# Kernel optimization log

Hardware: AMD Instinct MI355X
Metric: run time of the kernel (lower is better)

Reference implementation:

```python
import jax, jax.numpy as jnp
import numpy as np

B, S, D = 32, 512, 1024  # batch, seq_len, input_dim == output_dim


def setup_inputs() -> dict:
    key = jax.random.key(0)
    ks = jax.random.split(key, 13)
    std = 0.05  # tf.random_normal_initializer default stddev
    w = lambda k, shp: (jax.random.normal(k, shp, dtype=jnp.float32) * std)
    inp = {"seq_input_vec": jax.random.normal(ks[0], (B, S, D), dtype=jnp.float32)}
    names = ["Ui", "Wi", "Uf", "Wf", "Uo", "Wo", "Ug", "Wg"]
    for i, n in enumerate(names):
        inp[n] = w(ks[1 + i], (D, D))
    for n in ["bi", "bf", "bo", "bg"]:
        inp[n] = jnp.zeros((D,), dtype=jnp.float32)
    return inp


def reference(seq_input_vec, Ui, Wi, bi, Uf, Wf, bf, Uo, Wo, bo, Ug, Wg, bg):
    # seq_input_vec: [B, S, D]. Fuse the 4 input projections into one GEMM
    # over the whole sequence (mathematically identical to per-step matmuls).
    U = jnp.concatenate([Ui, Uf, Uo, Ug], axis=1)          # [D, 4D]
    W = jnp.concatenate([Wi, Wf, Wo, Wg], axis=1)          # [D, 4D]
    b = jnp.concatenate([bi, bf, bo, bg], axis=0)          # [4D]
    x_proj = jnp.einsum('bsd,de->sbe', seq_input_vec, U) + b  # [S, B, 4D]

    d = seq_input_vec.shape[-1]
    h0 = jnp.zeros((seq_input_vec.shape[0], d), dtype=seq_input_vec.dtype)
    c0 = jnp.zeros_like(h0)

    def step(carry, xp):
        c_prev, h_prev = carry
        z = xp + h_prev @ W                                 # [B, 4D]
        zi, zf, zo, zg = jnp.split(z, 4, axis=-1)
        i_t = jax.nn.sigmoid(zi)
        f_t = jax.nn.sigmoid(zf)
        o_t = jax.nn.sigmoid(zo)
        g_t = jnp.tanh(zg)
        # NOTE: original (nonstandard) math applies sigmoid to the cell update
        c_t = jax.nn.sigmoid(f_t * c_prev + i_t * g_t)
        h_t = jnp.tanh(c_t) * o_t
        return (c_t, h_t), h_t

    _, hs = jax.lax.scan(step, (c0, h0), x_proj)            # hs: [S, B, D]
    return jnp.transpose(hs, (1, 0, 2))                     # [B, S, D]
```

## Files before the change

### kernel.cpp

```cpp
#include <hip/hip_runtime.h>

typedef unsigned int u32;
typedef unsigned short u16;
typedef unsigned long long u64;
typedef __attribute__((ext_vector_type(8))) short short8;
typedef __attribute__((ext_vector_type(4))) float f32x4;
typedef __attribute__((ext_vector_type(4))) u32 u32x4;

#define SEQ 512
#define BATCH 32
#define DIM 1024
#define NB 128

#define OFF_XT    0ull
#define OFF_UBT   33554432ull
#define OFF_WG2   41943040ull
#define OFF_XPROJ 50331648ull
#define OFF_BIAS  184680448ull
#define OFF_SYNC  184696832ull

__device__ __forceinline__ float bf2f(u16 u) {
  union { u32 u; float f; } v; v.u = ((u32)u) << 16; return v.f;
}
__device__ __forceinline__ u16 f2bf(float f) {
  union { float f; u32 u; } v; v.f = f;
  u32 r = v.u + 0x7FFFu + ((v.u >> 16) & 1u);
  return (u16)(r >> 16);
}
__device__ __forceinline__ float tanh_fast(float x) {
  return 1.f - 2.f / (1.f + __expf(2.f * x));
}
__device__ __forceinline__ void gload_lds16(const u16* g, u16* l) {
  __builtin_amdgcn_global_load_lds(
      (const __attribute__((address_space(1))) u32*)g,
      (__attribute__((address_space(3))) u32*)l, 16, 0, 0);
}
__device__ __forceinline__ void gload_lds16_coh(const u16* g, u16* l) {
  __builtin_amdgcn_global_load_lds(
      (const __attribute__((address_space(1))) u32*)g,
      (__attribute__((address_space(3))) u32*)l, 16, 0, 17);
}

__global__ void k_init(float* biasc, u32* sync, const float* bi,
                       const float* bfv, const float* bo, const float* bg) {
  int i = blockIdx.x * 256 + threadIdx.x;
  if (i < 4096) {
    int g = i >> 10, c = i & 1023;
    const float* p = (g == 0) ? bi : (g == 1) ? bfv : (g == 2) ? bo : bg;
    biasc[i] = p[c];
  } else if (i < 8192) {
    sync[i - 4096] = 0u;
  }
}

__global__ void k_zero(u32x4* p) {
  p[blockIdx.x * 256 + threadIdx.x] = (u32x4){0u, 0u, 0u, 0u};
}

__global__ void k_prep_w(const float* Ui, const float* Wi, const float* Uf,
                         const float* Wf, const float* Uo, const float* Wo,
                         const float* Ug, const float* Wg, u16* Ubt, u16* Wg2) {
  __shared__ float tile[64][65];
  int bx = blockIdx.x;
  int mi = bx >> 8;
  int tt = bx & 255;
  int tr = tt >> 4, tc = tt & 15;
  const float* src;
  switch (mi) {
    case 0: src = Ui; break; case 1: src = Wi; break;
    case 2: src = Uf; break; case 3: src = Wf; break;
    case 4: src = Uo; break; case 5: src = Wo; break;
    case 6: src = Ug; break; default: src = Wg; break;
  }
  int g = mi >> 1;
  int d0 = tr * 64, c0 = tc * 64;
  int ty = threadIdx.x >> 6, tx = threadIdx.x & 63;
#pragma unroll
  for (int i = 0; i < 16; ++i) {
    int r = i * 4 + ty;
    tile[r][tx] = src[(size_t)(d0 + r) * 1024 + c0 + tx];
  }
  __syncthreads();
  if (mi & 1) {
#pragma unroll
    for (int i = 0; i < 16; ++i) {
      int cc = i * 4 + ty;
      int c_full = c0 + cc;
      int k = d0 + tx;
      int blk = c_full >> 3;
      int lane = (((k & 31) >> 3) << 4) + ((c_full & 3) << 2) + g;
      size_t idx = (size_t)blk * 32768 +
                   (size_t)(((k >> 5) * 2 + ((c_full & 7) >> 2)) * 64 + lane) * 8 +
                   (k & 7);
      Wg2[idx] = f2bf(tile[tx][cc]);
    }
  } else {
#pragma unroll
    for (int i = 0; i < 16; ++i) {
      int cc = i * 4 + ty;
      Ubt[(size_t)((g << 10) + c0 + cc) * 1024 + d0 + tx] = f2bf(tile[tx][cc]);
    }
  }
}

__global__ void k_prep_x(const float* __restrict__ X, u16* __restrict__ Xt) {
  int idx = blockIdx.x * 256 + threadIdx.x;
  int m = idx >> 8, d4 = (idx & 255) << 2;
  int s = m >> 5, b = m & 31;
  const float4* p = (const float4*)(X + (size_t)(b * SEQ + s) * DIM + d4);
  float4 v = *p;
  u16 o[4] = { f2bf(v.x), f2bf(v.y), f2bf(v.z), f2bf(v.w) };
  *(ushort4*)(Xt + (size_t)m * DIM + d4) = *(ushort4*)o;
}

__global__ __launch_bounds__(256) void k_gemm(const u16* __restrict__ Xt,
                                              const u16* __restrict__ Ubt,
                                              const float* __restrict__ biasc,
                                              u16* __restrict__ xp2) {
  __shared__ u16 As[128 * 32];
  __shared__ u16 Bs[128 * 32];
  __shared__ u16 cbuf[4][16][8][32];
  int tid = threadIdx.x;
  int w = tid >> 6, l = tid & 63;
  int n0 = blockIdx.x * 128, m0 = blockIdx.y * 128;
  int wm = w >> 1, wn = w & 1;
  int lrow = l & 15, lq = l >> 4;
  f32x4 acc[4][4] = {};
  for (int kt = 0; kt < 32; ++kt) {
    int k0 = kt * 32;
    __syncthreads();
#pragma unroll
    for (int is = 0; is < 2; ++is) {
      int c = is * 256 + w * 64 + l;
      int row = c >> 2, kg = c & 3;
      gload_lds16(Xt + (size_t)(m0 + row) * 1024 + k0 + kg * 8, As + c * 8);
      gload_lds16(Ubt + (size_t)(n0 + row) * 1024 + k0 + kg * 8, Bs + c * 8);
    }
    __syncthreads();
    short8 af[4], bfr[4];
#pragma unroll
    for (int mt = 0; mt < 4; ++mt)
      af[mt] = *(const short8*)(As + (wm * 64 + mt * 16 + lrow) * 32 + lq * 8);
#pragma unroll
    for (int nt = 0; nt < 4; ++nt)
      bfr[nt] = *(const short8*)(Bs + (wn * 64 + nt * 16 + lrow) * 32 + lq * 8);
#pragma unroll
    for (int mt = 0; mt < 4; ++mt)
#pragma unroll
      for (int nt = 0; nt < 4; ++nt)
        acc[mt][nt] = __builtin_amdgcn_mfma_f32_16x16x32_bf16(
            af[mt], bfr[nt], acc[mt][nt], 0, 0, 0);
  }
#pragma unroll
  for (int nt = 0; nt < 4; ++nt) {
    int lc = wn * 64 + nt * 16 + lrow;
    float bv = biasc[n0 + lc];
#pragma unroll
    for (int mt = 0; mt < 4; ++mt) {
#pragma unroll
      for (int r = 0; r < 4; ++r) {
        int lr = wm * 64 + mt * 16 + lq * 4 + r;
        cbuf[lr >> 5][lc >> 3][lrow & 7][lr & 31] = f2bf(acc[mt][nt][r] + bv);
      }
    }
  }
  __syncthreads();
  int s0 = m0 >> 5, blkd0 = (n0 & 1023) >> 3, gb = (n0 >> 10) * 256;
  const u16* cb = &cbuf[0][0][0][0];
#pragma unroll
  for (int i = 0; i < 8; ++i) {
    int u = i * 256 + tid;
    int r_ = u >> 5, w_ = u & 31;
    u32x4 v = *(const u32x4*)(cb + u * 8);
    *(u32x4*)(xp2 + (size_t)((s0 + (r_ >> 4)) * 128 + blkd0 + (r_ & 15)) * 1024 +
              gb + w_ * 8) = v;
  }
}

__global__ __launch_bounds__(256, 1) void k_rec(const u16* __restrict__ Wg2,
                                                const u16* __restrict__ xp2,
                                                u16* hX, const u16* __restrict__ h0,
                                                u32* sync) {
  __shared__ u16 Hs[32768];
  __shared__ u16 XPs[2][1024];
  int tid = threadIdx.x;
  int w = tid >> 6, l = tid & 63;
  int mt = w >> 1, nt = w & 1;
  int blk = blockIdx.x;
  int q = l >> 4, b15 = l & 15;

  short8 wf[32];
#pragma unroll
  for (int kt = 0; kt < 32; ++kt)
    wf[kt] = *(const short8*)(Wg2 + (size_t)blk * 32768 + (kt * 2 + mt) * 512 +
                              l * 8);
  if (tid < 128)
    gload_lds16(xp2 + (size_t)blk * 1024 + tid * 8, XPs[0] + tid * 8);
  asm volatile("s_waitcnt vmcnt(0)" ::: "memory");
  __builtin_amdgcn_sched_barrier(0);

  int hoff = (((blk >> 2) * 2 + nt) * 64 + (blk & 3) * 16 + b15) * 8 + mt * 4 + q;
  int xoff = (mt * 4 + q) * 32 + nt * 16 + b15;
  float c_reg = 0.f;
  __syncthreads();

  for (int s = 0; s < SEQ; ++s) {
    {
      u32 tgt = (u32)s;
      int guard = 0;
      for (;;) {
        u32 a = __hip_atomic_load(sync + l * 32, __ATOMIC_RELAXED,
                                  __HIP_MEMORY_SCOPE_AGENT);
        u32 b = __hip_atomic_load(sync + (64 + l) * 32, __ATOMIC_RELAXED,
                                  __HIP_MEMORY_SCOPE_AGENT);
        if (a >= tgt && b >= tgt) break;
        __builtin_amdgcn_s_sleep(1);
        if (++guard > 1000000) break;
      }
    }
    asm volatile("" ::: "memory");
    __builtin_amdgcn_sched_barrier(0);

    const u16* hs = (s == 0) ? h0 : (hX + (size_t)(s - 1) * 32768);
#pragma unroll
    for (int it = 0; it < 16; ++it)
      gload_lds16_coh(hs + (it * 256 + tid) * 8, Hs + (it * 256 + tid) * 8);

    f32x4 a0 = {0.f, 0.f, 0.f, 0.f}, a1 = {0.f, 0.f, 0.f, 0.f};
    asm volatile("s_waitcnt vmcnt(8)" ::: "memory");
    __builtin_amdgcn_sched_barrier(0);
    __builtin_amdgcn_s_barrier();
    __builtin_amdgcn_sched_barrier(0);
#pragma unroll
    for (int kt = 0; kt < 16; kt += 2) {
      short8 b0 = *(const short8*)(Hs + (kt * 2 + nt) * 512 + l * 8);
      short8 b1 = *(const short8*)(Hs + ((kt + 1) * 2 + nt) * 512 + l * 8);
      a0 = __builtin_amdgcn_mfma_f32_16x16x32_bf16(wf[kt], b0, a0, 0, 0, 0);
      a1 = __builtin_amdgcn_mfma_f32_16x16x32_bf16(wf[kt + 1], b1, a1, 0, 0, 0);
    }
    asm volatile("s_waitcnt vmcnt(0)" ::: "memory");
    __builtin_amdgcn_sched_barrier(0);
    __builtin_amdgcn_s_barrier();
    __builtin_amdgcn_sched_barrier(0);
#pragma unroll
    for (int kt = 16; kt < 32; kt += 2) {
      short8 b0 = *(const short8*)(Hs + (kt * 2 + nt) * 512 + l * 8);
      short8 b1 = *(const short8*)(Hs + ((kt + 1) * 2 + nt) * 512 + l * 8);
      a0 = __builtin_amdgcn_mfma_f32_16x16x32_bf16(wf[kt], b0, a0, 0, 0, 0);
      a1 = __builtin_amdgcn_mfma_f32_16x16x32_bf16(wf[kt + 1], b1, a1, 0, 0, 0);
    }
    f32x4 z4 = a0 + a1;

    const u16* xp = XPs[s & 1];
    float zi = z4[0] + bf2f(xp[xoff]);
    float zf = z4[1] + bf2f(xp[256 + xoff]);
    float zo = z4[2] + bf2f(xp[512 + xoff]);
    float zg = z4[3] + bf2f(xp[768 + xoff]);
    float ig = 1.f / (1.f + __expf(-zi));
    float fg = 1.f / (1.f + __expf(-zf));
    float og = 1.f / (1.f + __expf(-zo));
    float gg = tanh_fast(zg);
    c_reg = 1.f / (1.f + __expf(-(fg * c_reg + ig * gg)));
    float h = tanh_fast(c_reg) * og;

    __hip_atomic_store(hX + (size_t)s * 32768 + hoff, f2bf(h),
                       __ATOMIC_RELAXED, __HIP_MEMORY_SCOPE_AGENT);
    __syncthreads();
    if (tid == 0)
      __hip_atomic_store(sync + blk * 32, (u32)(s + 1), __ATOMIC_RELAXED,
                         __HIP_MEMORY_SCOPE_AGENT);
    {
      int sp = (s + 1 < SEQ) ? s + 1 : s;
      if (tid < 128)
        gload_lds16(xp2 + ((size_t)sp * 128 + blk) * 1024 + tid * 8,
                    XPs[(s + 1) & 1] + tid * 8);
    }
  }
}

__global__ void k_out(const u16* __restrict__ hx, float* __restrict__ out) {
  int t = blockIdx.x * 256 + threadIdx.x;
  int d0 = (t & 127) << 3;
  int rem = t >> 7;
  int s = rem & 511, b = rem >> 9;
  int kt = d0 >> 5, jg = (d0 & 31) >> 3, ct = b >> 4;
  const u16* src = hx + (size_t)s * 32768 +
                   (size_t)(((kt * 2 + ct) * 64 + jg * 16 + (b & 15)) * 8);
  ushort4 v0 = *(const ushort4*)src;
  ushort4 v1 = *(const ushort4*)(src + 4);
  float4 o0 = { bf2f(v0.x), bf2f(v0.y), bf2f(v0.z), bf2f(v0.w) };
  float4 o1 = { bf2f(v1.x), bf2f(v1.y), bf2f(v1.z), bf2f(v1.w) };
  float* dst = out + (size_t)(b * SEQ + s) * DIM + d0;
  *(float4*)dst = o0;
  *(float4*)(dst + 4) = o1;
}

extern "C" void kernel_launch(void* const* d_in, const int* in_sizes, int n_in,
                              void* d_out, int out_size, void* d_ws,
                              size_t ws_size, hipStream_t stream) {
  const float* X   = (const float*)d_in[0];
  const float* Ui  = (const float*)d_in[1];
  const float* Wi  = (const float*)d_in[2];
  const float* Uf  = (const float*)d_in[3];
  const float* Wf  = (const float*)d_in[4];
  const float* Uo  = (const float*)d_in[5];
  const float* Wo  = (const float*)d_in[6];
  const float* Ug  = (const float*)d_in[7];
  const float* Wg  = (const float*)d_in[8];
  const float* bi  = (const float*)d_in[9];
  const float* bfv = (const float*)d_in[10];
  const float* bo  = (const float*)d_in[11];
  const float* bg  = (const float*)d_in[12];
  char* ws = (char*)d_ws;
  u16* Xt      = (u16*)(ws + OFF_XT);
  u16* Ubt     = (u16*)(ws + OFF_UBT);
  u16* Wg2     = (u16*)(ws + OFF_WG2);
  u16* xp2     = (u16*)(ws + OFF_XPROJ);
  float* biasc = (float*)(ws + OFF_BIAS);
  u32* sync    = (u32*)(ws + OFF_SYNC);
  float* out   = (float*)d_out;

  k_init<<<32, 256, 0, stream>>>(biasc, sync, bi, bfv, bo, bg);
  k_prep_w<<<2048, 256, 0, stream>>>(Ui, Wi, Uf, Wf, Uo, Wo, Ug, Wg, Ubt, Wg2);
  k_prep_x<<<16384, 256, 0, stream>>>(X, Xt);
  k_gemm<<<dim3(32, 128), 256, 0, stream>>>(Xt, Ubt, biasc, xp2);
  k_zero<<<16, 256, 0, stream>>>((u32x4*)Ubt);
  k_rec<<<NB, 256, 0, stream>>>(Wg2, xp2, Xt, Ubt, sync);
  k_out<<<8192, 256, 0, stream>>>(Xt, out);
}
```

Before: 1.789 ms.

## Use per-wave sync flags and direct register h loads in recurrent kernel

The recurrent kernel now keeps its W slice in LDS rather than in registers. Each wave loads the h fragments it needs straight into registers with coherent global loads, in a three-buffer software pipeline, which removes the shared Hs staging and the block-wide barriers. Synchronisation moves from one flag per block to one flag per wave, and each wave polls only the 256 flags of its half of the batch, so waves no longer wait on a block-level __syncthreads. The trade-off is more poll loads per wave and W fragment reads from LDS on every step, and per-wave memory ordering now depends on the vmcnt waits being placed correctly.

```diff
diff --git a/kernel.cpp b/kernel.cpp
--- a/kernel.cpp
+++ b/kernel.cpp
@@ -34,11 +34,6 @@
   __builtin_amdgcn_global_load_lds(
       (const __attribute__((address_space(1))) u32*)g,
       (__attribute__((address_space(3))) u32*)l, 16, 0, 0);
-}
-__device__ __forceinline__ void gload_lds16_coh(const u16* g, u16* l) {
-  __builtin_amdgcn_global_load_lds(
-      (const __attribute__((address_space(1))) u32*)g,
-      (__attribute__((address_space(3))) u32*)l, 16, 0, 17);
 }
 
 __global__ void k_init(float* biasc, u32* sync, const float* bi,
@@ -48,7 +43,7 @@
     int g = i >> 10, c = i & 1023;
     const float* p = (g == 0) ? bi : (g == 1) ? bfv : (g == 2) ? bo : bg;
     biasc[i] = p[c];
-  } else if (i < 8192) {
+  } else if (i < 4096 + 2048) {
     sync[i - 4096] = 0u;
   }
 }
@@ -181,39 +176,61 @@
                                                 const u16* __restrict__ xp2,
                                                 u16* hX, const u16* __restrict__ h0,
                                                 u32* sync) {
-  __shared__ u16 Hs[32768];
-  __shared__ u16 XPs[2][1024];
+  __shared__ u16 Ws[32768];
+  __shared__ u16 XPs[4][2][512];
   int tid = threadIdx.x;
   int w = tid >> 6, l = tid & 63;
   int mt = w >> 1, nt = w & 1;
   int blk = blockIdx.x;
   int q = l >> 4, b15 = l & 15;
 
-  short8 wf[32];
-#pragma unroll
-  for (int kt = 0; kt < 32; ++kt)
-    wf[kt] = *(const short8*)(Wg2 + (size_t)blk * 32768 + (kt * 2 + mt) * 512 +
-                              l * 8);
-  if (tid < 128)
-    gload_lds16(xp2 + (size_t)blk * 1024 + tid * 8, XPs[0] + tid * 8);
-  asm volatile("s_waitcnt vmcnt(0)" ::: "memory");
-  __builtin_amdgcn_sched_barrier(0);
-
+#pragma unroll
+  for (int it = 0; it < 16; ++it)
+    gload_lds16(Wg2 + (size_t)blk * 32768 + (it * 256 + tid) * 8,
+                Ws + (it * 256 + tid) * 8);
+  int xsrc = (l >> 4) * 256 + (mt * 4 + ((l & 15) >> 2)) * 32 + (l & 3) * 8;
+  gload_lds16(xp2 + (size_t)blk * 1024 + xsrc, &XPs[w][0][l * 8]);
+  int xrd = q * 32 + nt * 16 + b15;
   int hoff = (((blk >> 2) * 2 + nt) * 64 + (blk & 3) * 16 + b15) * 8 + mt * 4 + q;
-  int xoff = (mt * 4 + q) * 32 + nt * 16 + b15;
+  int fid = nt * 256 + blk * 2 + mt;
+  const u32* pollbase = sync + (size_t)nt * 256 * 4;
   float c_reg = 0.f;
   __syncthreads();
+
+  u32x4 qA[8], qB[8], qC[8];
+#define ISSUE8(BUF, T0)                                                     \
+  _Pragma("unroll")                                                         \
+  for (int t = 0; t < 8; ++t) {                                             \
+    asm volatile("global_load_dwordx4 %0, %1, off sc0 sc1"                  \
+                 : "=v"(BUF[t])                                             \
+                 : "v"(hs + (((T0) + t) * 2 + nt) * 512 + l * 8));          \
+  }
+#define MFMA8(BUF, KT0)                                                     \
+  _Pragma("unroll")                                                         \
+  for (int t = 0; t < 8; ++t) {                                             \
+    int kt = (KT0) + t;                                                     \
+    short8 wfr = *(const short8*)(Ws + (kt * 2 + mt) * 512 + l * 8);        \
+    short8 bfr = __builtin_bit_cast(short8, BUF[t]);                        \
+    if (t & 1)                                                              \
+      a1 = __builtin_amdgcn_mfma_f32_16x16x32_bf16(wfr, bfr, a1, 0, 0, 0);  \
+    else                                                                    \
+      a0 = __builtin_amdgcn_mfma_f32_16x16x32_bf16(wfr, bfr, a0, 0, 0, 0);  \
+  }
 
   for (int s = 0; s < SEQ; ++s) {
     {
       u32 tgt = (u32)s;
       int guard = 0;
       for (;;) {
-        u32 a = __hip_atomic_load(sync + l * 32, __ATOMIC_RELAXED,
-                                  __HIP_MEMORY_SCOPE_AGENT);
-        u32 b = __hip_atomic_load(sync + (64 + l) * 32, __ATOMIC_RELAXED,
-                                  __HIP_MEMORY_SCOPE_AGENT);
-        if (a >= tgt && b >= tgt) break;
+        u32 f0 = __hip_atomic_load(pollbase + (l) * 4, __ATOMIC_RELAXED,
+                                   __HIP_MEMORY_SCOPE_AGENT);
+        u32 f1 = __hip_atomic_load(pollbase + (64 + l) * 4, __ATOMIC_RELAXED,
+                                   __HIP_MEMORY_SCOPE_AGENT);
+        u32 f2 = __hip_atomic_load(pollbase + (128 + l) * 4, __ATOMIC_RELAXED,
+                                   __HIP_MEMORY_SCOPE_AGENT);
+        u32 f3 = __hip_atomic_load(pollbase + (192 + l) * 4, __ATOMIC_RELAXED,
+                                   __HIP_MEMORY_SCOPE_AGENT);
+        if (f0 >= tgt && f1 >= tgt && f2 >= tgt && f3 >= tgt) break;
         __builtin_amdgcn_s_sleep(1);
         if (++guard > 1000000) break;
       }
@@ -222,40 +239,34 @@
     __builtin_amdgcn_sched_barrier(0);
 
     const u16* hs = (s == 0) ? h0 : (hX + (size_t)(s - 1) * 32768);
-#pragma unroll
-    for (int it = 0; it < 16; ++it)
-      gload_lds16_coh(hs + (it * 256 + tid) * 8, Hs + (it * 256 + tid) * 8);
+    {
+      int sp = (s + 1 < SEQ) ? s + 1 : s;
+      gload_lds16(xp2 + ((size_t)sp * 128 + blk) * 1024 + xsrc,
+                  &XPs[w][(s + 1) & 1][l * 8]);
+    }
+    ISSUE8(qA, 0) ISSUE8(qB, 8) ISSUE8(qC, 16)
 
     f32x4 a0 = {0.f, 0.f, 0.f, 0.f}, a1 = {0.f, 0.f, 0.f, 0.f};
+    asm volatile("s_waitcnt vmcnt(16)" ::: "memory");
+    __builtin_amdgcn_sched_barrier(0);
+    MFMA8(qA, 0)
+    ISSUE8(qA, 24)
+    asm volatile("s_waitcnt vmcnt(16)" ::: "memory");
+    __builtin_amdgcn_sched_barrier(0);
+    MFMA8(qB, 8)
     asm volatile("s_waitcnt vmcnt(8)" ::: "memory");
     __builtin_amdgcn_sched_barrier(0);
-    __builtin_amdgcn_s_barrier();
-    __builtin_amdgcn_sched_barrier(0);
-#pragma unroll
-    for (int kt = 0; kt < 16; kt += 2) {
-      short8 b0 = *(const short8*)(Hs + (kt * 2 + nt) * 512 + l * 8);
-      short8 b1 = *(const short8*)(Hs + ((kt + 1) * 2 + nt) * 512 + l * 8);
-      a0 = __builtin_amdgcn_mfma_f32_16x16x32_bf16(wf[kt], b0, a0, 0, 0, 0);
-      a1 = __builtin_amdgcn_mfma_f32_16x16x32_bf16(wf[kt + 1], b1, a1, 0, 0, 0);
-    }
+    MFMA8(qC, 16)
     asm volatile("s_waitcnt vmcnt(0)" ::: "memory");
     __builtin_amdgcn_sched_barrier(0);
-    __builtin_amdgcn_s_barrier();
-    __builtin_amdgcn_sched_barrier(0);
-#pragma unroll
-    for (int kt = 16; kt < 32; kt += 2) {
-      short8 b0 = *(const short8*)(Hs + (kt * 2 + nt) * 512 + l * 8);
-      short8 b1 = *(const short8*)(Hs + ((kt + 1) * 2 + nt) * 512 + l * 8);
-      a0 = __builtin_amdgcn_mfma_f32_16x16x32_bf16(wf[kt], b0, a0, 0, 0, 0);
-      a1 = __builtin_amdgcn_mfma_f32_16x16x32_bf16(wf[kt + 1], b1, a1, 0, 0, 0);
-    }
+    MFMA8(qA, 24)
     f32x4 z4 = a0 + a1;
 
-    const u16* xp = XPs[s & 1];
-    float zi = z4[0] + bf2f(xp[xoff]);
-    float zf = z4[1] + bf2f(xp[256 + xoff]);
-    float zo = z4[2] + bf2f(xp[512 + xoff]);
-    float zg = z4[3] + bf2f(xp[768 + xoff]);
+    const u16* xp = XPs[w][s & 1];
+    float zi = z4[0] + bf2f(xp[xrd]);
+    float zf = z4[1] + bf2f(xp[128 + xrd]);
+    float zo = z4[2] + bf2f(xp[256 + xrd]);
+    float zg = z4[3] + bf2f(xp[384 + xrd]);
     float ig = 1.f / (1.f + __expf(-zi));
     float fg = 1.f / (1.f + __expf(-zf));
     float og = 1.f / (1.f + __expf(-zo));
@@ -265,17 +276,14 @@
 
     __hip_atomic_store(hX + (size_t)s * 32768 + hoff, f2bf(h),
                        __ATOMIC_RELAXED, __HIP_MEMORY_SCOPE_AGENT);
-    __syncthreads();
-    if (tid == 0)
-      __hip_atomic_store(sync + blk * 32, (u32)(s + 1), __ATOMIC_RELAXED,
+    asm volatile("s_waitcnt vmcnt(0)" ::: "memory");
+    __builtin_amdgcn_sched_barrier(0);
+    if (l == 0)
+      __hip_atomic_store(sync + fid * 4, (u32)(s + 1), __ATOMIC_RELAXED,
                          __HIP_MEMORY_SCOPE_AGENT);
-    {
-      int sp = (s + 1 < SEQ) ? s + 1 : s;
-      if (tid < 128)
-        gload_lds16(xp2 + ((size_t)sp * 128 + blk) * 1024 + tid * 8,
-                    XPs[(s + 1) & 1] + tid * 8);
-    }
-  }
+  }
+#undef ISSUE8
+#undef MFMA8
 }
 
 __global__ void k_out(const u16* __restrict__ hx, float* __restrict__ out) {
@@ -320,7 +328,7 @@
   u32* sync    = (u32*)(ws + OFF_SYNC);
   float* out   = (float*)d_out;
 
-  k_init<<<32, 256, 0, stream>>>(biasc, sync, bi, bfv, bo, bg);
+  k_init<<<24, 256, 0, stream>>>(biasc, sync, bi, bfv, bo, bg);
   k_prep_w<<<2048, 256, 0, stream>>>(Ui, Wi, Uf, Wf, Uo, Wo, Ug, Wg, Ubt, Wg2);
   k_prep_x<<<16384, 256, 0, stream>>>(X, Xt);
   k_gemm<<<dim3(32, 128), 256, 0, stream>>>(Xt, Ubt, biasc, xp2);
```

Result: slower. 2.789 ms (+55.9%).
